# Performance work log

Measured on AMD Instinct MI355X. Metric: run time of the kernel, lower is better.

The kernel has to match this reference:

```python
import jax, jax.numpy as jnp
import numpy as np

K = 7          # involution kernel size
PAD = 3        # (K-1)//2
G = 4          # groups = out_channels // group_channels
GC = 16        # group_channels
EPS = 1e-5     # BatchNorm eps


def _bn(x, g, b, m, v):
    # eval-mode BatchNorm2d over channel dim of NCHW
    scale = g / jnp.sqrt(v + EPS)
    return x * scale[:, None, None] + (b - m * scale)[:, None, None]


def _conv1x1(x, w, b=None):
    y = jnp.einsum('bchw,oc->bohw', x, w)
    if b is not None:
        y = y + b[:, None, None]
    return y


def _gelu(x):
    return jax.nn.gelu(x, approximate=False)  # torch nn.GELU default (erf)


def _involution(x, wr, gr, br, mr, vr, ws, bs):
    # kernel-generation branch: 1x1 reduce -> BN -> ReLU -> 1x1 span
    r = jax.nn.relu(_bn(_conv1x1(x, wr), gr, br, mr, vr))
    w = _conv1x1(r, ws, bs)                       # [B, G*K*K, H, W]
    B, _, H, W = w.shape
    w = w.reshape(B, G, K * K, H, W)
    # unfold x into KxK patches (channel-major then row-major kernel pos, matching nn.Unfold)
    xp = jnp.pad(x, ((0, 0), (0, 0), (PAD, PAD), (PAD, PAD)))
    patches = jnp.stack([xp[:, :, i:i + H, j:j + W]
                         for i in range(K) for j in range(K)], axis=2)  # [B, C, KK, H, W]
    patches = patches.reshape(B, G, GC, K * K, H, W)
    out = jnp.einsum('bgkhw,bgckhw->bgchw', w, patches)  # per-pixel dynamic kernel apply
    return out.reshape(B, G * GC, H, W)


def setup_inputs() -> dict:
    key = jax.random.key(0)
    ks = jax.random.split(key, 24)
    B, Cin, Cout, H, W = 4, 32, 64, 128, 128
    red = Cout // 4
    n = lambda k, s, sc: jax.random.normal(k, s, jnp.float32) * sc
    u = lambda k, s: jax.random.uniform(k, s, jnp.float32, 0.5, 1.5)
    inp = {
        'x': n(ks[0], (B, Cin, H, W), 1.0),
        'w1': n(ks[1], (Cout, Cin), 0.15),
        # involution: reduce conv + BN, span conv
        'wr': n(ks[2], (red, Cout), 0.12), 'gr': u(ks[3], (red,)), 'br': n(ks[4], (red,), 0.05),
        'mr': n(ks[5], (red,), 0.05), 'vr': u(ks[6], (red,)),
        'ws': n(ks[7], (K * K * G, red), 0.1), 'bs': n(ks[8], (K * K * G,), 0.02),
        # BN after involution
        'g1': u(ks[9], (Cout,)), 'b1': n(ks[10], (Cout,), 0.05),
        'm1': n(ks[11], (Cout,), 0.05), 'v1': u(ks[12], (Cout,)),
        # convblock2
        'w2': n(ks[13], (Cout, Cout), 0.12),
        'g2': u(ks[14], (Cout,)), 'b2': n(ks[15], (Cout,), 0.05),
        'm2': n(ks[16], (Cout,), 0.05), 'v2': u(ks[17], (Cout,)),
        # mapping (residual projection) conv has bias=True by default
        'wm': n(ks[18], (Cout, Cin), 0.15), 'bmap': n(ks[19], (Cout,), 0.02),
        'gm': u(ks[20], (Cout,)), 'betam': n(ks[21], (Cout,), 0.05),
        'mm': n(ks[22], (Cout,), 0.05), 'vm': u(ks[23], (Cout,)),
    }
    return inp


def reference(x, w1, wr, gr, br, mr, vr, ws, bs, g1, b1, m1, v1,
              w2, g2, b2, m2, v2, wm, bmap, gm, betam, mm, vm):
    x1 = _gelu(_conv1x1(x, w1))                                  # convblock
    x1 = _gelu(_bn(_involution(x1, wr, gr, br, mr, vr, ws, bs),
                   g1, b1, m1, v1))                              # involution + BN + GELU
    x1 = _bn(_conv1x1(x1, w2), g2, b2, m2, v2)                   # convblock2
    skip = _bn(_conv1x1(x, wm, bmap), gm, betam, mm, vm)         # mapping (Cin != Cout)
    return _gelu(x1 + skip)
```

## Files before the change

kernel.cpp:

```cpp
#include <hip/hip_runtime.h>
#include <hip/hip_bf16.h>
#include <math.h>

#define HW    16384
#define Bsz   4
#define CIN   32
#define COUT  64
#define RED   16
#define KKN   49
#define GG    4
#define PW    134
#define NHALO 25152
#define NZB   99
#define NPXB  1024

typedef __hip_bfloat16 bf16;
typedef __attribute__((ext_vector_type(8))) short bf16x8;
typedef __attribute__((ext_vector_type(4))) float f32x4;

__device__ __forceinline__ float gelu_f(float x) {
    return 0.5f * x * (1.0f + erff(x * 0.70710678118654752f));
}
__device__ __forceinline__ void unpack_bf2(unsigned u, float& lo, float& hi) {
    lo = __uint_as_float(u << 16);
    hi = __uint_as_float(u & 0xffff0000u);
}
__device__ __forceinline__ unsigned pack_bf2(float lo, float hi) {
    unsigned a = __float_as_uint(lo), b = __float_as_uint(hi);
    a += 0x7fff + ((a >> 16) & 1);
    b += 0x7fff + ((b >> 16) & 1);
    return (a >> 16) | (b & 0xffff0000u);
}
__device__ __forceinline__ unsigned short bf16r(float v) {
    unsigned a = __float_as_uint(v);
    a += 0x7fff + ((a >> 16) & 1);
    return (unsigned short)(a >> 16);
}

#define OFF_RBUF  9437184
#define OFF_PAR   22020096
#define OFF_XBF   22085632
#define PSHC_F 16
#define PSMV_F 80
#define PSC1_F 144
#define PSH1_F 208
#define BCAT 12288

__global__ __launch_bounds__(256, 4) void k1_all(
    const float* __restrict__ x, const float* __restrict__ w1,
    const float* __restrict__ wr, const float* __restrict__ gr,
    const float* __restrict__ br, const float* __restrict__ mr,
    const float* __restrict__ vr,
    const float* __restrict__ g1, const float* __restrict__ b1,
    const float* __restrict__ m1, const float* __restrict__ v1,
    const float* __restrict__ w2, const float* __restrict__ g2,
    const float* __restrict__ b2, const float* __restrict__ m2,
    const float* __restrict__ v2,
    const float* __restrict__ wm, const float* __restrict__ bmap,
    const float* __restrict__ gm, const float* __restrict__ betam,
    const float* __restrict__ mm, const float* __restrict__ vm,
    char* __restrict__ parb, unsigned* __restrict__ x1pad,
    unsigned short* __restrict__ xbf, float* __restrict__ rbuf)
{
    __shared__ float x1f[4][16][65];
    int bid = blockIdx.x, t = threadIdx.x;

    if (bid >= NPXB) {
        int hb = bid - NPXB;
        if (hb < NZB) {
            unsigned i = (unsigned)hb * 256u + (unsigned)t;
            if (i < NHALO) {
                unsigned plane = i / 1572u;
                unsigned rem = i - plane * 1572u;
                unsigned row, col;
                if (rem < 804u) {
                    unsigned rr = rem / 134u;
                    col = rem - rr * 134u;
                    row = rr < 3u ? rr : rr + 128u;
                } else {
                    unsigned r2 = rem - 804u;
                    unsigned rr = r2 / 6u;
                    unsigned cc = r2 - rr * 6u;
                    row = rr + 3u;
                    col = cc < 3u ? cc : cc + 128u;
                }
                uint4* q = (uint4*)x1pad + ((size_t)(plane * PW + row) * PW + col) * 2;
                q[0] = make_uint4(0u, 0u, 0u, 0u);
                q[1] = make_uint4(0u, 0u, 0u, 0u);
            }
        } else {
            float* parf = (float*)parb;
            unsigned short* wcat = (unsigned short*)(parb + BCAT);
            for (int i = t; i < 64 * 96; i += 256) {
                int o = i / 96, c = i - o * 96;
                float v;
                if (c < 64) {
                    float s2 = g2[o] * rsqrtf(v2[o] + 1e-5f);
                    float sm = gm[o] * rsqrtf(vm[o] + 1e-5f);
                    v = w2[o * COUT + c] * (s2 / sm);
                } else {
                    v = wm[o * CIN + (c - 64)];
                }
                wcat[i] = bf16r(v);
            }
            if (t < 64) {
                float s2 = g2[t] * rsqrtf(v2[t] + 1e-5f);
                float sm = gm[t] * rsqrtf(vm[t] + 1e-5f);
                parf[PSHC_F + t] = (b2[t] - m2[t] * s2) + (betam[t] + (bmap[t] - mm[t]) * sm);
                parf[PSMV_F + t] = sm;
                float s1 = g1[t] * rsqrtf(v1[t] + 1e-5f);
                parf[PSC1_F + t] = s1;
                parf[PSH1_F + t] = b1[t] - m1[t] * s1;
            }
        }
        return;
    }

    int lane = t & 63;
    int wave = t >> 6;
    int m15 = lane & 15, quad = lane >> 4;
    int base_gpx = bid * 64 + wave * 16;
    int b   = base_gpx >> 14;
    int px0 = base_gpx & (HW - 1);

    int gpx = base_gpx + m15;
    int p   = gpx & (HW - 1);
    unsigned apk[4];
#pragma unroll
    for (int d = 0; d < 4; ++d) {
        float lo = x[((size_t)(b * CIN + quad * 8 + 2 * d)) * HW + p];
        float hi = x[((size_t)(b * CIN + quad * 8 + 2 * d + 1)) * HW + p];
        apk[d] = pack_bf2(lo, hi);
    }
    union BU { uint4 q; bf16x8 v; };
    BU au; au.q = make_uint4(apk[0], apk[1], apk[2], apk[3]);
    bf16x8 Af = au.v;
    *(uint4*)&xbf[(size_t)gpx * 32 + quad * 8] = au.q;

    f32x4 acc[4];
#pragma unroll
    for (int nt = 0; nt < 4; ++nt) {
        int o = nt * 16 + m15;
        unsigned bpk[4];
#pragma unroll
        for (int d = 0; d < 4; ++d) {
            float lo = w1[o * CIN + quad * 8 + 2 * d];
            float hi = w1[o * CIN + quad * 8 + 2 * d + 1];
            bpk[d] = pack_bf2(lo, hi);
        }
        BU bu; bu.q = make_uint4(bpk[0], bpk[1], bpk[2], bpk[3]);
        f32x4 z = {0.f, 0.f, 0.f, 0.f};
        acc[nt] = __builtin_amdgcn_mfma_f32_16x16x32_bf16(Af, bu.v, z, 0, 0, 0);
    }
#pragma unroll
    for (int nt = 0; nt < 4; ++nt)
#pragma unroll
        for (int reg = 0; reg < 4; ++reg)
            x1f[wave][quad * 4 + reg][nt * 16 + m15] = gelu_f(acc[nt][reg]);

    __syncthreads();

    {
        int pxl = lane >> 2, g = lane & 3;
        int pp = px0 + pxl, h = pp >> 7, w = pp & 127;
        unsigned pk[8];
#pragma unroll
        for (int d = 0; d < 8; ++d)
            pk[d] = pack_bf2(x1f[wave][pxl][g * 16 + 2 * d],
                             x1f[wave][pxl][g * 16 + 2 * d + 1]);
        unsigned* xo = x1pad +
            ((size_t)((b * GG + g) * PW + (h + 3)) * PW + (w + 3)) * 8;
        *(uint4*)xo       = make_uint4(pk[0], pk[1], pk[2], pk[3]);
        *(uint4*)(xo + 4) = make_uint4(pk[4], pk[5], pk[6], pk[7]);
    }

    float sc  = gr[m15] * rsqrtf(vr[m15] + 1e-5f);
    float rsh = br[m15] - mr[m15] * sc;
    f32x4 racc = {0.f, 0.f, 0.f, 0.f};
#pragma unroll
    for (int kt = 0; kt < 2; ++kt) {
        bf16x8 A2, B2;
#pragma unroll
        for (int j = 0; j < 8; ++j) {
            A2[j] = (short)bf16r(x1f[wave][m15][kt * 32 + quad * 8 + j]);
            B2[j] = (short)bf16r(wr[m15 * 64 + kt * 32 + quad * 8 + j] * sc);
        }
        racc = __builtin_amdgcn_mfma_f32_16x16x32_bf16(A2, B2, racc, 0, 0, 0);
    }
#pragma unroll
    for (int reg = 0; reg < 4; ++reg) {
        int gp = base_gpx + quad * 4 + reg;
        rbuf[(size_t)gp * 16 + m15] = fmaxf(racc[reg] + rsh, 0.f);
    }
}

__global__ __launch_bounds__(256, 2) void k34_fused(
    const unsigned* __restrict__ x1pad, const float* __restrict__ rbuf,
    const float* __restrict__ wsp, const float* __restrict__ bsp,
    const char* __restrict__ parb, const unsigned short* __restrict__ xbf,
    float* __restrict__ out)
{
    __shared__ unsigned short x2t[2][64][88];

    const float* par = (const float*)parb;
    int t = threadIdx.x;
    int b    = blockIdx.x >> 7;
    int tile = blockIdx.x & 127;
    int R  = tile >> 1;
    int Cc = tile & 1;
    int h0 = 2 * R;

    {
        int c = t & 63;
        int g = __builtin_amdgcn_readfirstlane(t >> 6);
        int w0 = Cc * 64 + c;
        int p0 = h0 * 128 + w0;
        int bg = b * GG + g;

        float r0[RED], r1[RED];
        {
            const float4* rp = (const float4*)&rbuf[((size_t)b * HW + p0) * 16];
            float4 a0 = rp[0], a1 = rp[1], a2 = rp[2], a3 = rp[3];
            r0[0]=a0.x; r0[1]=a0.y; r0[2]=a0.z; r0[3]=a0.w;
            r0[4]=a1.x; r0[5]=a1.y; r0[6]=a1.z; r0[7]=a1.w;
            r0[8]=a2.x; r0[9]=a2.y; r0[10]=a2.z; r0[11]=a2.w;
            r0[12]=a3.x; r0[13]=a3.y; r0[14]=a3.z; r0[15]=a3.w;
            const float4* rq = (const float4*)&rbuf[((size_t)b * HW + p0 + 128) * 16];
            float4 c0 = rq[0], c1 = rq[1], c2 = rq[2], c3 = rq[3];
            r1[0]=c0.x; r1[1]=c0.y; r1[2]=c0.z; r1[3]=c0.w;
            r1[4]=c1.x; r1[5]=c1.y; r1[6]=c1.z; r1[7]=c1.w;
            r1[8]=c2.x; r1[9]=c2.y; r1[10]=c2.z; r1[11]=c2.w;
            r1[12]=c3.x; r1[13]=c3.y; r1[14]=c3.z; r1[15]=c3.w;
        }

        const float* wrow = wsp + g * KKN * RED;
        const float* brow = bsp + g * KKN;

        float acc0[RED], acc1[RED];
#pragma unroll
        for (int cc = 0; cc < RED; ++cc) { acc0[cc] = 0.f; acc1[cc] = 0.f; }

#pragma unroll 1
        for (int ir = 0; ir < 8; ++ir) {
            const unsigned* rowp = x1pad +
                ((size_t)(bg * PW + h0 + ir) * PW + w0) * 8;
#pragma unroll 1
            for (int j = 0; j < 7; ++j) {
                const unsigned* tp = rowp + (size_t)j * 8;
                uint4 A = *(const uint4*)tp;
                uint4 B = *(const uint4*)(tp + 4);
                float f[16];
                unpack_bf2(A.x, f[0], f[1]);   unpack_bf2(A.y, f[2], f[3]);
                unpack_bf2(A.z, f[4], f[5]);   unpack_bf2(A.w, f[6], f[7]);
                unpack_bf2(B.x, f[8], f[9]);   unpack_bf2(B.y, f[10], f[11]);
                unpack_bf2(B.z, f[12], f[13]); unpack_bf2(B.w, f[14], f[15]);
                if (ir < 7) {
                    int k = ir * 7 + j;
                    const float* wk = wrow + k * RED;
                    float s = brow[k];
#pragma unroll
                    for (int jj = 0; jj < RED; ++jj) s += r0[jj] * wk[jj];
#pragma unroll
                    for (int cc = 0; cc < RED; ++cc) acc0[cc] += s * f[cc];
                }
                if (ir > 0) {
                    int k = (ir - 1) * 7 + j;
                    const float* wk = wrow + k * RED;
                    float s = brow[k];
#pragma unroll
                    for (int jj = 0; jj < RED; ++jj) s += r1[jj] * wk[jj];
#pragma unroll
                    for (int cc = 0; cc < RED; ++cc) acc1[cc] += s * f[cc];
                }
            }
        }

        unsigned pk0[8], pk1[8];
#pragma unroll
        for (int d = 0; d < 8; ++d) {
            int ch0 = g * RED + 2 * d, ch1 = ch0 + 1;
            float sA = par[PSC1_F + ch0], sB = par[PSC1_F + ch1];
            float hA = par[PSH1_F + ch0], hB = par[PSH1_F + ch1];
            pk0[d] = pack_bf2(gelu_f(sA * acc0[2 * d]     + hA),
                              gelu_f(sB * acc0[2 * d + 1] + hB));
            pk1[d] = pack_bf2(gelu_f(sA * acc1[2 * d]     + hA),
                              gelu_f(sB * acc1[2 * d + 1] + hB));
        }
        unsigned* xo0 = (unsigned*)&x2t[0][c][g * RED];
        *(uint4*)xo0       = make_uint4(pk0[0], pk0[1], pk0[2], pk0[3]);
        *(uint4*)(xo0 + 4) = make_uint4(pk0[4], pk0[5], pk0[6], pk0[7]);
        unsigned* xo1 = (unsigned*)&x2t[1][c][g * RED];
        *(uint4*)xo1       = make_uint4(pk1[0], pk1[1], pk1[2], pk1[3]);
        *(uint4*)(xo1 + 4) = make_uint4(pk1[4], pk1[5], pk1[6], pk1[7]);
    }

    __syncthreads();

    {
        int lane = t & 63, wave = t >> 6;
        int m15  = lane & 15;
        int quad = lane >> 4;
        int pxl0 = wave * 16;

        const unsigned short* wcat = (const unsigned short*)(parb + BCAT);

        bf16x8 Bf[3][4];
#pragma unroll
        for (int kt = 0; kt < 3; ++kt)
#pragma unroll
            for (int nt = 0; nt < 4; ++nt)
                Bf[kt][nt] = *(const bf16x8*)&wcat[(nt * 16 + m15) * 96 + kt * 32 + quad * 8];

#pragma unroll 1
        for (int rr = 0; rr < 2; ++rr) {
            int pbase = (h0 + rr) * 128 + Cc * 64;

            bf16x8 Af[3];
            Af[0] = *(const bf16x8*)&x2t[rr][pxl0 + m15][quad * 8];
            Af[1] = *(const bf16x8*)&x2t[rr][pxl0 + m15][32 + quad * 8];
            Af[2] = *(const bf16x8*)&xbf[((size_t)(b * HW + pbase + pxl0 + m15)) * 32 + quad * 8];

            f32x4 acc[4];
#pragma unroll
            for (int nt = 0; nt < 4; ++nt) acc[nt] = (f32x4){0.f, 0.f, 0.f, 0.f};
#pragma unroll
            for (int kt = 0; kt < 3; ++kt)
#pragma unroll
                for (int nt = 0; nt < 4; ++nt)
                    acc[nt] = __builtin_amdgcn_mfma_f32_16x16x32_bf16(
                        Af[kt], Bf[kt][nt], acc[nt], 0, 0, 0);

#pragma unroll
            for (int nt = 0; nt < 4; ++nt) {
                int o = nt * 16 + m15;
                float smv = par[PSMV_F + o], sh = par[PSHC_F + o];
                float* op = out + (size_t)(b * COUT + o) * HW + pbase + pxl0 + quad * 4;
#pragma unroll
                for (int reg = 0; reg < 4; ++reg)
                    op[reg] = gelu_f(smv * acc[nt][reg] + sh);
            }
        }
    }
}

extern "C" void kernel_launch(void* const* d_in, const int* in_sizes, int n_in,
                              void* d_out, int out_size, void* d_ws, size_t ws_size,
                              hipStream_t stream) {
    const float* x    = (const float*)d_in[0];
    const float* w1   = (const float*)d_in[1];
    const float* wr   = (const float*)d_in[2];
    const float* gr   = (const float*)d_in[3];
    const float* br   = (const float*)d_in[4];
    const float* mr   = (const float*)d_in[5];
    const float* vr   = (const float*)d_in[6];
    const float* wsp  = (const float*)d_in[7];
    const float* bsp  = (const float*)d_in[8];
    const float* g1   = (const float*)d_in[9];
    const float* b1   = (const float*)d_in[10];
    const float* m1   = (const float*)d_in[11];
    const float* v1   = (const float*)d_in[12];
    const float* w2   = (const float*)d_in[13];
    const float* g2   = (const float*)d_in[14];
    const float* b2   = (const float*)d_in[15];
    const float* m2   = (const float*)d_in[16];
    const float* v2   = (const float*)d_in[17];
    const float* wm   = (const float*)d_in[18];
    const float* bmap = (const float*)d_in[19];
    const float* gm   = (const float*)d_in[20];
    const float* betam= (const float*)d_in[21];
    const float* mm   = (const float*)d_in[22];
    const float* vm   = (const float*)d_in[23];

    unsigned*       x1pad = (unsigned*)d_ws;
    float*          rbuf  = (float*)((char*)d_ws + OFF_RBUF);
    char*           parb  = (char*)d_ws + OFF_PAR;
    unsigned short* xbf   = (unsigned short*)((char*)d_ws + OFF_XBF);

    k1_all<<<NPXB + NZB + 1, 256, 0, stream>>>(
        x, w1, wr, gr, br, mr, vr, g1, b1, m1, v1,
        w2, g2, b2, m2, v2, wm, bmap, gm, betam, mm, vm,
        parb, x1pad, xbf, rbuf);
    k34_fused<<<Bsz * (HW / 128), 256, 0, stream>>>(
        x1pad, rbuf, wsp, bsp, parb, xbf, (float*)d_out);
}
```

Before: 169.8 us.

## Process one pixel per thread in involution kernel to raise occupancy

Each block of the fused involution/convblock2 kernel now handles 64 pixels in one row instead of a 2-row pair. Previously each loaded patch tap was reused across two vertically adjacent pixels. Dropping that pair halves the accumulator and register footprint, allows launch bounds of 4 blocks per SM, doubles the grid and loads all 7 taps of a kernel row together for more memory-level parallelism. The cost is that 8-row loads now become 7 rows per pixel with no sharing, so global and cache traffic for x1pad rises by about 1.75x.

```diff
diff --git a/kernel.cpp b/kernel.cpp
--- a/kernel.cpp
+++ b/kernel.cpp
@@ -194,104 +194,84 @@
     }
 }
 
-__global__ __launch_bounds__(256, 2) void k34_fused(
+__global__ __launch_bounds__(256, 4) void k34_fused(
     const unsigned* __restrict__ x1pad, const float* __restrict__ rbuf,
     const float* __restrict__ wsp, const float* __restrict__ bsp,
     const char* __restrict__ parb, const unsigned short* __restrict__ xbf,
     float* __restrict__ out)
 {
-    __shared__ unsigned short x2t[2][64][88];
+    __shared__ unsigned short x2t[64][88];
 
     const float* par = (const float*)parb;
     int t = threadIdx.x;
-    int b    = blockIdx.x >> 7;
-    int tile = blockIdx.x & 127;
-    int R  = tile >> 1;
-    int Cc = tile & 1;
-    int h0 = 2 * R;
+    int b = blockIdx.x >> 8;
+    int pxblk = (blockIdx.x & 255) << 6;
 
     {
-        int c = t & 63;
+        int pxl = t & 63;
         int g = __builtin_amdgcn_readfirstlane(t >> 6);
-        int w0 = Cc * 64 + c;
-        int p0 = h0 * 128 + w0;
+        int p = pxblk + pxl;
+        int h = p >> 7, w0 = p & 127;
         int bg = b * GG + g;
 
-        float r0[RED], r1[RED];
+        float r[RED];
         {
-            const float4* rp = (const float4*)&rbuf[((size_t)b * HW + p0) * 16];
-            float4 a0 = rp[0], a1 = rp[1], a2 = rp[2], a3 = rp[3];
-            r0[0]=a0.x; r0[1]=a0.y; r0[2]=a0.z; r0[3]=a0.w;
-            r0[4]=a1.x; r0[5]=a1.y; r0[6]=a1.z; r0[7]=a1.w;
-            r0[8]=a2.x; r0[9]=a2.y; r0[10]=a2.z; r0[11]=a2.w;
-            r0[12]=a3.x; r0[13]=a3.y; r0[14]=a3.z; r0[15]=a3.w;
-            const float4* rq = (const float4*)&rbuf[((size_t)b * HW + p0 + 128) * 16];
-            float4 c0 = rq[0], c1 = rq[1], c2 = rq[2], c3 = rq[3];
-            r1[0]=c0.x; r1[1]=c0.y; r1[2]=c0.z; r1[3]=c0.w;
-            r1[4]=c1.x; r1[5]=c1.y; r1[6]=c1.z; r1[7]=c1.w;
-            r1[8]=c2.x; r1[9]=c2.y; r1[10]=c2.z; r1[11]=c2.w;
-            r1[12]=c3.x; r1[13]=c3.y; r1[14]=c3.z; r1[15]=c3.w;
+            const float4* rp = (const float4*)&rbuf[((size_t)b * HW + p) * 16];
+            float4 r0 = rp[0], r1 = rp[1], r2 = rp[2], r3 = rp[3];
+            r[0]=r0.x; r[1]=r0.y; r[2]=r0.z; r[3]=r0.w;
+            r[4]=r1.x; r[5]=r1.y; r[6]=r1.z; r[7]=r1.w;
+            r[8]=r2.x; r[9]=r2.y; r[10]=r2.z; r[11]=r2.w;
+            r[12]=r3.x; r[13]=r3.y; r[14]=r3.z; r[15]=r3.w;
         }
 
         const float* wrow = wsp + g * KKN * RED;
         const float* brow = bsp + g * KKN;
-
-        float acc0[RED], acc1[RED];
-#pragma unroll
-        for (int cc = 0; cc < RED; ++cc) { acc0[cc] = 0.f; acc1[cc] = 0.f; }
+        const unsigned* base = x1pad + ((size_t)(bg * PW + h) * PW + w0) * 8;
+
+        float acc[RED];
+#pragma unroll
+        for (int c = 0; c < RED; ++c) acc[c] = 0.f;
 
 #pragma unroll 1
-        for (int ir = 0; ir < 8; ++ir) {
-            const unsigned* rowp = x1pad +
-                ((size_t)(bg * PW + h0 + ir) * PW + w0) * 8;
-#pragma unroll 1
+        for (int i = 0; i < 7; ++i) {
+            const unsigned* rowp = base + (size_t)i * (PW * 8);
+            uint4 A[7], Bv[7];
+#pragma unroll
             for (int j = 0; j < 7; ++j) {
                 const unsigned* tp = rowp + (size_t)j * 8;
-                uint4 A = *(const uint4*)tp;
-                uint4 B = *(const uint4*)(tp + 4);
-                float f[16];
-                unpack_bf2(A.x, f[0], f[1]);   unpack_bf2(A.y, f[2], f[3]);
-                unpack_bf2(A.z, f[4], f[5]);   unpack_bf2(A.w, f[6], f[7]);
-                unpack_bf2(B.x, f[8], f[9]);   unpack_bf2(B.y, f[10], f[11]);
-                unpack_bf2(B.z, f[12], f[13]); unpack_bf2(B.w, f[14], f[15]);
-                if (ir < 7) {
-                    int k = ir * 7 + j;
-                    const float* wk = wrow + k * RED;
-                    float s = brow[k];
-#pragma unroll
-                    for (int jj = 0; jj < RED; ++jj) s += r0[jj] * wk[jj];
-#pragma unroll
-                    for (int cc = 0; cc < RED; ++cc) acc0[cc] += s * f[cc];
-                }
-                if (ir > 0) {
-                    int k = (ir - 1) * 7 + j;
-                    const float* wk = wrow + k * RED;
-                    float s = brow[k];
-#pragma unroll
-                    for (int jj = 0; jj < RED; ++jj) s += r1[jj] * wk[jj];
-#pragma unroll
-                    for (int cc = 0; cc < RED; ++cc) acc1[cc] += s * f[cc];
-                }
-            }
-        }
-
-        unsigned pk0[8], pk1[8];
+                A[j]  = *(const uint4*)tp;
+                Bv[j] = *(const uint4*)(tp + 4);
+            }
+#pragma unroll
+            for (int j = 0; j < 7; ++j) {
+                int k = i * 7 + j;
+                const float* wk = wrow + k * RED;
+                float s = brow[k];
+#pragma unroll
+                for (int jj = 0; jj < RED; ++jj) s += r[jj] * wk[jj];
+                float lo, hi;
+                unpack_bf2(A[j].x, lo, hi); acc[0] += s*lo; acc[1] += s*hi;
+                unpack_bf2(A[j].y, lo, hi); acc[2] += s*lo; acc[3] += s*hi;
+                unpack_bf2(A[j].z, lo, hi); acc[4] += s*lo; acc[5] += s*hi;
+                unpack_bf2(A[j].w, lo, hi); acc[6] += s*lo; acc[7] += s*hi;
+                unpack_bf2(Bv[j].x, lo, hi); acc[8] += s*lo; acc[9] += s*hi;
+                unpack_bf2(Bv[j].y, lo, hi); acc[10]+= s*lo; acc[11]+= s*hi;
+                unpack_bf2(Bv[j].z, lo, hi); acc[12]+= s*lo; acc[13]+= s*hi;
+                unpack_bf2(Bv[j].w, lo, hi); acc[14]+= s*lo; acc[15]+= s*hi;
+            }
+        }
+
+        unsigned pk[8];
 #pragma unroll
         for (int d = 0; d < 8; ++d) {
             int ch0 = g * RED + 2 * d, ch1 = ch0 + 1;
-            float sA = par[PSC1_F + ch0], sB = par[PSC1_F + ch1];
-            float hA = par[PSH1_F + ch0], hB = par[PSH1_F + ch1];
-            pk0[d] = pack_bf2(gelu_f(sA * acc0[2 * d]     + hA),
-                              gelu_f(sB * acc0[2 * d + 1] + hB));
-            pk1[d] = pack_bf2(gelu_f(sA * acc1[2 * d]     + hA),
-                              gelu_f(sB * acc1[2 * d + 1] + hB));
-        }
-        unsigned* xo0 = (unsigned*)&x2t[0][c][g * RED];
-        *(uint4*)xo0       = make_uint4(pk0[0], pk0[1], pk0[2], pk0[3]);
-        *(uint4*)(xo0 + 4) = make_uint4(pk0[4], pk0[5], pk0[6], pk0[7]);
-        unsigned* xo1 = (unsigned*)&x2t[1][c][g * RED];
-        *(uint4*)xo1       = make_uint4(pk1[0], pk1[1], pk1[2], pk1[3]);
-        *(uint4*)(xo1 + 4) = make_uint4(pk1[4], pk1[5], pk1[6], pk1[7]);
+            float v0 = gelu_f(par[PSC1_F + ch0] * acc[2 * d]     + par[PSH1_F + ch0]);
+            float v1 = gelu_f(par[PSC1_F + ch1] * acc[2 * d + 1] + par[PSH1_F + ch1]);
+            pk[d] = pack_bf2(v0, v1);
+        }
+        unsigned* xo = (unsigned*)&x2t[pxl][g * RED];
+        *(uint4*)xo       = make_uint4(pk[0], pk[1], pk[2], pk[3]);
+        *(uint4*)(xo + 4) = make_uint4(pk[4], pk[5], pk[6], pk[7]);
     }
 
     __syncthreads();
@@ -301,6 +281,7 @@
         int m15  = lane & 15;
         int quad = lane >> 4;
         int pxl0 = wave * 16;
+        int px0  = pxblk + pxl0;
 
         const unsigned short* wcat = (const unsigned short*)(parb + BCAT);
 
@@ -311,34 +292,29 @@
             for (int nt = 0; nt < 4; ++nt)
                 Bf[kt][nt] = *(const bf16x8*)&wcat[(nt * 16 + m15) * 96 + kt * 32 + quad * 8];
 
-#pragma unroll 1
-        for (int rr = 0; rr < 2; ++rr) {
-            int pbase = (h0 + rr) * 128 + Cc * 64;
-
-            bf16x8 Af[3];
-            Af[0] = *(const bf16x8*)&x2t[rr][pxl0 + m15][quad * 8];
-            Af[1] = *(const bf16x8*)&x2t[rr][pxl0 + m15][32 + quad * 8];
-            Af[2] = *(const bf16x8*)&xbf[((size_t)(b * HW + pbase + pxl0 + m15)) * 32 + quad * 8];
-
-            f32x4 acc[4];
-#pragma unroll
-            for (int nt = 0; nt < 4; ++nt) acc[nt] = (f32x4){0.f, 0.f, 0.f, 0.f};
-#pragma unroll
-            for (int kt = 0; kt < 3; ++kt)
-#pragma unroll
-                for (int nt = 0; nt < 4; ++nt)
-                    acc[nt] = __builtin_amdgcn_mfma_f32_16x16x32_bf16(
-                        Af[kt], Bf[kt][nt], acc[nt], 0, 0, 0);
-
-#pragma unroll
-            for (int nt = 0; nt < 4; ++nt) {
-                int o = nt * 16 + m15;
-                float smv = par[PSMV_F + o], sh = par[PSHC_F + o];
-                float* op = out + (size_t)(b * COUT + o) * HW + pbase + pxl0 + quad * 4;
-#pragma unroll
-                for (int reg = 0; reg < 4; ++reg)
-                    op[reg] = gelu_f(smv * acc[nt][reg] + sh);
-            }
+        bf16x8 Af[3];
+        Af[0] = *(const bf16x8*)&x2t[pxl0 + m15][quad * 8];
+        Af[1] = *(const bf16x8*)&x2t[pxl0 + m15][32 + quad * 8];
+        Af[2] = *(const bf16x8*)&xbf[((size_t)(b * HW + px0 + m15)) * 32 + quad * 8];
+
+        f32x4 acc[4];
+#pragma unroll
+        for (int nt = 0; nt < 4; ++nt) acc[nt] = (f32x4){0.f, 0.f, 0.f, 0.f};
+#pragma unroll
+        for (int kt = 0; kt < 3; ++kt)
+#pragma unroll
+            for (int nt = 0; nt < 4; ++nt)
+                acc[nt] = __builtin_amdgcn_mfma_f32_16x16x32_bf16(
+                    Af[kt], Bf[kt][nt], acc[nt], 0, 0, 0);
+
+#pragma unroll
+        for (int nt = 0; nt < 4; ++nt) {
+            int o = nt * 16 + m15;
+            float smv = par[PSMV_F + o], sh = par[PSHC_F + o];
+            float* op = out + (size_t)(b * COUT + o) * HW + px0 + quad * 4;
+#pragma unroll
+            for (int reg = 0; reg < 4; ++reg)
+                op[reg] = gelu_f(smv * acc[nt][reg] + sh);
         }
     }
 }
@@ -380,6 +356,6 @@
         x, w1, wr, gr, br, mr, vr, g1, b1, m1, v1,
         w2, g2, b2, m2, v2, wm, bmap, gm, betam, mm, vm,
         parb, x1pad, xbf, rbuf);
-    k34_fused<<<Bsz * (HW / 128), 256, 0, stream>>>(
+    k34_fused<<<Bsz * GG * HW / 256, 256, 0, stream>>>(
         x1pad, rbuf, wsp, bsp, parb, xbf, (float*)d_out);
 }
```

Measured after the change: 221.0 us. 30.2% more time.
